# Kernel tuning notes

Hardware: AMD Instinct MI355X
Metric: run time of the kernel (lower is better)

The kernel has to match this reference:

```python
import jax, jax.numpy as jnp
import numpy as np

N = 100000
E = 1600000
IN_C, HID_C, OUT_C = 64, 64, 32


def setup_inputs() -> dict:
    key = jax.random.key(0)
    ks = jax.random.split(key, 8)
    x = jax.random.normal(ks[0], (N, IN_C), dtype=jnp.float32)
    edge_index = jax.random.randint(ks[1], (2, E), 0, N, dtype=jnp.int64)
    # GCNConv weights (glorot-ish scale) and biases
    W1 = jax.random.normal(ks[2], (IN_C, HID_C), dtype=jnp.float32) / np.sqrt(IN_C)
    b1 = jnp.zeros((HID_C,), dtype=jnp.float32)
    W2 = jax.random.normal(ks[3], (HID_C, HID_C), dtype=jnp.float32) / np.sqrt(HID_C)
    b2 = jnp.zeros((HID_C,), dtype=jnp.float32)
    Wlin = jax.random.normal(ks[4], (HID_C, OUT_C), dtype=jnp.float32) / np.sqrt(HID_C)
    blin = jnp.zeros((OUT_C,), dtype=jnp.float32)
    return {"x": x, "edge_index": edge_index, "W1": W1, "b1": b1,
            "W2": W2, "b2": b2, "Wlin": Wlin, "blin": blin}


def _gcn_norm(edge_index):
    # PyG GCNConv default: add self-loops, symmetric normalization.
    loop = jnp.arange(N, dtype=edge_index.dtype)
    row = jnp.concatenate([edge_index[0], loop])  # source nodes [E+N]
    col = jnp.concatenate([edge_index[1], loop])  # target nodes [E+N]
    deg = jax.ops.segment_sum(jnp.ones_like(col, dtype=jnp.float32), col,
                              num_segments=N)
    dinv = jnp.where(deg > 0, deg ** -0.5, 0.0)
    norm = dinv[row] * dinv[col]  # [E+N]
    return row, col, norm


def _gcn_conv(h, W, b, row, col, norm):
    h = h @ W                                  # [N, F_out]
    msg = h[row] * norm[:, None]               # gather + scale, [E+N, F_out]
    out = jax.ops.segment_sum(msg, col, num_segments=N)  # scatter-add
    return out + b


def reference(x, edge_index, W1, b1, W2, b2, Wlin, blin):
    row, col, norm = _gcn_norm(edge_index)
    h = jax.nn.relu(_gcn_conv(x, W1, b1, row, col, norm))
    h = jax.nn.relu(_gcn_conv(h, W2, b2, row, col, norm))
    return h @ Wlin + blin
```

## Files before the change

### kernel.cpp

```cpp
#include <hip/hip_runtime.h>
#include <hip/hip_fp16.h>

#define IN_C 64
#define HID_C 64
#define OUT_C 32
#define S_NODES  512
#define S_CAP  12288
#define CHUNK_E 2048

typedef _Float16 f16_t;
typedef f16_t f16x2 __attribute__((ext_vector_type(2)));

__device__ __forceinline__ float dot2(unsigned int a, f16x2 b, float c) {
#if __has_builtin(__builtin_amdgcn_fdot2)
    return __builtin_amdgcn_fdot2(*(f16x2*)&a, b, c, false);
#else
    float2 af = __half22float2(*(__half2*)&a);
    __half2 bh; *(f16x2*)&bh = b;
    float2 bf = __half22float2(bh);
    return fmaf(af.x, bf.x, fmaf(af.y, bf.y, c));
#endif
}

__global__ void detect_fmt(const int* ei32, int* flag, int n_check) {
    __shared__ int s_any;
    if (threadIdx.x == 0) s_any = 0;
    __syncthreads();
    int any = 0;
    for (int i = threadIdx.x; i < n_check; i += blockDim.x) {
        if (ei32[2 * i + 1] != 0) any = 1;
    }
    if (any) atomicOr(&s_any, 1);
    __syncthreads();
    if (threadIdx.x == 0) *flag = (s_any == 0) ? 1 : 0;
}

__device__ __forceinline__ int ld_edge(const void* ei, int idx, int is64) {
    if (is64) return (int)((const long long*)ei)[idx];
    return ((const int*)ei)[idx];
}

__global__ __launch_bounds__(256) void bin_edges(const void* ei, int E, const int* flag,
                                                 int* bcur, int NB,
                                                 int* __restrict__ staging) {
    __shared__ int cnt[256], boff[256], lcur[256], gbase[256];
    __shared__ int stg[CHUNK_E];
    __shared__ int s_is64;
    int tid = threadIdx.x;
    if (tid == 0) s_is64 = *flag;
    cnt[tid] = 0;
    __syncthreads();
    int is64 = s_is64;
    int e0 = blockIdx.x * CHUNK_E;
    int e1 = min(E, e0 + CHUNK_E);
    for (int e = e0 + tid; e < e1; e += 256) {
        int dst = ld_edge(ei, E + e, is64);
        atomicAdd(&cnt[dst >> 9], 1);
    }
    __syncthreads();
    int v = cnt[tid];
    gbase[tid] = v;
    __syncthreads();
    for (int o = 1; o < 256; o <<= 1) {
        int u = (tid >= o) ? gbase[tid - o] : 0;
        __syncthreads();
        gbase[tid] += u;
        __syncthreads();
    }
    boff[tid] = gbase[tid] - v;
    lcur[tid] = boff[tid];
    __syncthreads();
    for (int e = e0 + tid; e < e1; e += 256) {
        int src = ld_edge(ei, e, is64);
        int dst = ld_edge(ei, E + e, is64);
        int p = atomicAdd(&lcur[dst >> 9], 1);
        stg[p] = src | ((dst & 511) << 17);
    }
    __syncthreads();
    if (tid < NB && cnt[tid] > 0) gbase[tid] = atomicAdd(&bcur[tid], cnt[tid]);
    __syncthreads();
    int sw = tid >> 4, sl = tid & 15;
    for (int b = sw; b < NB; b += 16) {
        int c = cnt[b];
        if (c == 0) continue;
        int o = boff[b], g = gbase[b];
        size_t gb = (size_t)b * S_CAP;
        for (int j = sl; j < c; j += 16) {
            if (g + j < S_CAP) staging[gb + g + j] = stg[o + j];
        }
    }
}

__global__ void scan_bcur(const int* __restrict__ bcur, int* __restrict__ bbase,
                          int* __restrict__ offs, int nb, int n) {
    __shared__ int s[256];
    int tid = threadIdx.x;
    int v = (tid < nb) ? min(bcur[tid], S_CAP) : 0;
    s[tid] = v;
    __syncthreads();
    for (int o = 1; o < 256; o <<= 1) {
        int u = (tid >= o) ? s[tid - o] : 0;
        __syncthreads();
        s[tid] += u;
        __syncthreads();
    }
    if (tid < nb) bbase[tid] = s[tid] - v;
    if (tid == 255) offs[n] = s[255];
}

__global__ __launch_bounds__(256) void place_fine(const int* __restrict__ staging,
                                                  const int* __restrict__ bcur,
                                                  const int* __restrict__ bbase,
                                                  int* __restrict__ offs,
                                                  float* __restrict__ dinv,
                                                  int* __restrict__ rec, int N) {
    __shared__ int sdeg[S_NODES];
    __shared__ int tsum[256];
    __shared__ int curs[S_NODES];
    int tid = threadIdx.x;
    int base = blockIdx.x * S_NODES;
    int nn = min(S_NODES, N - base);
    int cnt = min(bcur[blockIdx.x], S_CAP);
    size_t sb = (size_t)blockIdx.x * S_CAP;
    sdeg[tid] = 0;
    sdeg[tid + 256] = 0;
    __syncthreads();
    for (int j = tid; j < cnt; j += 256) atomicAdd(&sdeg[staging[sb + j] >> 17], 1);
    __syncthreads();
    int d0 = sdeg[2 * tid], d1 = sdeg[2 * tid + 1];
    tsum[tid] = d0 + d1;
    __syncthreads();
    for (int o = 1; o < 256; o <<= 1) {
        int v = (tid >= o) ? tsum[tid - o] : 0;
        __syncthreads();
        tsum[tid] += v;
        __syncthreads();
    }
    int pre = bbase[blockIdx.x] + ((tid == 0) ? 0 : tsum[tid - 1]);
    curs[2 * tid] = pre;
    curs[2 * tid + 1] = pre + d0;
    if (2 * tid < nn) {
        offs[base + 2 * tid] = pre;
        dinv[base + 2 * tid] = rsqrtf((float)(d0 + 1));
    }
    if (2 * tid + 1 < nn) {
        offs[base + 2 * tid + 1] = pre + d0;
        dinv[base + 2 * tid + 1] = rsqrtf((float)(d1 + 1));
    }
    __syncthreads();
    for (int j = tid; j < cnt; j += 256) {
        int pk = staging[sb + j];
        int p = atomicAdd(&curs[pk >> 17], 1);
        rec[p] = pk & 0x1FFFF;
    }
}

__global__ __launch_bounds__(256) void gemm64(const void* __restrict__ in, int in_is_f32,
                                              const float* __restrict__ W,
                                              unsigned short* __restrict__ out,
                                              const float* __restrict__ dinv, int n) {
    __shared__ uint2 sA[32 * 16];
    int tid = threadIdx.x;
    int lane = tid & 63, wave = tid >> 6;
    f16x2 w2[32];
#pragma unroll
    for (int k = 0; k < 32; k++) {
        f16x2 p;
        p.x = (f16_t)W[(2 * k) * 64 + lane];
        p.y = (f16_t)W[(2 * k + 1) * 64 + lane];
        w2[k] = p;
    }
    int base = blockIdx.x * 32;
    if (in_is_f32) {
        const float2* A2 = (const float2*)in;
        int lim = n * 32;
        for (int i = tid; i < 1024; i += 256) {
            int gi = base * 32 + i;
            float2 v = (gi < lim) ? A2[gi] : make_float2(0.f, 0.f);
            ((__half2*)sA)[i] = __floats2half2_rn(v.x, v.y);
        }
    } else {
        const uint2* A2 = (const uint2*)in;
        int lim = n * 16;
        for (int i = tid; i < 512; i += 256) {
            int gi = base * 16 + i;
            sA[i] = (gi < lim) ? A2[gi] : make_uint2(0u, 0u);
        }
    }
    __syncthreads();
    int r0 = base + wave * 8;
    int r1 = min(r0 + 8, n);
    for (int r = r0; r < r1; r++) {
        int rr = r - base;
        float a0 = 0.f, a1 = 0.f;
#pragma unroll
        for (int j = 0; j < 16; j++) {
            uint2 u = sA[rr * 16 + j];
            a0 = dot2(u.x, w2[2 * j], a0);
            a1 = dot2(u.y, w2[2 * j + 1], a1);
        }
        __half hv = __float2half_rn((a0 + a1) * dinv[r]);
        out[(size_t)r * 64 + lane] = *(unsigned short*)&hv;
    }
}

__global__ void aggregate(const unsigned short* __restrict__ t,
                          const int* __restrict__ offs, const int* __restrict__ rec,
                          const float* __restrict__ dinv, const float* __restrict__ bias,
                          unsigned short* __restrict__ acc, int n) {
    int wave = (blockIdx.x * blockDim.x + threadIdx.x) >> 6;
    int lane = threadIdx.x & 63;
    if (wave >= n) return;
    int g = lane >> 3;
    int gl = lane & 7;
    int beg = offs[wave], end = offs[wave + 1];
    int m = end - beg + 1;
    const uint4* t4 = (const uint4*)t;
    float s[8] = {0.f, 0.f, 0.f, 0.f, 0.f, 0.f, 0.f, 0.f};
    for (int i = 0; i < m; i += 32) {
        int srcs[4];
        float ws[4];
#pragma unroll
        for (int u = 0; u < 4; u++) {
            int it = i + u * 8 + g;
            srcs[u] = (it == 0) ? wave : ((it < m) ? rec[beg + it - 1] : wave);
            ws[u] = (it < m) ? 1.f : 0.f;
        }
        uint4 vs[4];
#pragma unroll
        for (int u = 0; u < 4; u++) vs[u] = t4[(size_t)srcs[u] * 8 + gl];
#pragma unroll
        for (int u = 0; u < 4; u++) {
            float w = ws[u];
            float2 f0 = __half22float2(*(__half2*)&vs[u].x);
            float2 f1 = __half22float2(*(__half2*)&vs[u].y);
            float2 f2 = __half22float2(*(__half2*)&vs[u].z);
            float2 f3 = __half22float2(*(__half2*)&vs[u].w);
            s[0] = fmaf(f0.x, w, s[0]);
            s[1] = fmaf(f0.y, w, s[1]);
            s[2] = fmaf(f1.x, w, s[2]);
            s[3] = fmaf(f1.y, w, s[3]);
            s[4] = fmaf(f2.x, w, s[4]);
            s[5] = fmaf(f2.y, w, s[5]);
            s[6] = fmaf(f3.x, w, s[6]);
            s[7] = fmaf(f3.y, w, s[7]);
        }
    }
#pragma unroll
    for (int k = 0; k < 8; k++) {
        s[k] += __shfl_xor(s[k], 8);
        s[k] += __shfl_xor(s[k], 16);
        s[k] += __shfl_xor(s[k], 32);
    }
    if (g == 0) {
        float d = dinv[wave];
        const float4* b4 = (const float4*)bias;
        float4 bb0 = b4[gl * 2], bb1 = b4[gl * 2 + 1];
        float o0 = fmaxf(fmaf(s[0], d, bb0.x), 0.f);
        float o1 = fmaxf(fmaf(s[1], d, bb0.y), 0.f);
        float o2 = fmaxf(fmaf(s[2], d, bb0.z), 0.f);
        float o3 = fmaxf(fmaf(s[3], d, bb0.w), 0.f);
        float o4 = fmaxf(fmaf(s[4], d, bb1.x), 0.f);
        float o5 = fmaxf(fmaf(s[5], d, bb1.y), 0.f);
        float o6 = fmaxf(fmaf(s[6], d, bb1.z), 0.f);
        float o7 = fmaxf(fmaf(s[7], d, bb1.w), 0.f);
        __half2 p0 = __floats2half2_rn(o0, o1);
        __half2 p1 = __floats2half2_rn(o2, o3);
        __half2 p2 = __floats2half2_rn(o4, o5);
        __half2 p3 = __floats2half2_rn(o6, o7);
        ((uint4*)acc)[(size_t)wave * 8 + gl] =
            make_uint4(*(unsigned int*)&p0, *(unsigned int*)&p1,
                       *(unsigned int*)&p2, *(unsigned int*)&p3);
    }
}

__global__ __launch_bounds__(256) void gemm32(const unsigned short* __restrict__ in,
                                              const float* __restrict__ W,
                                              const float* __restrict__ b,
                                              float* __restrict__ out, int n) {
    __shared__ uint2 sA[32 * 16];
    int tid = threadIdx.x;
    int lane = tid & 63, wave = tid >> 6;
    int c = lane & 31;
    f16x2 w2[32];
#pragma unroll
    for (int k = 0; k < 32; k++) {
        f16x2 p;
        p.x = (f16_t)W[(2 * k) * 32 + c];
        p.y = (f16_t)W[(2 * k + 1) * 32 + c];
        w2[k] = p;
    }
    float bl = b[c];
    int base = blockIdx.x * 32;
    const uint2* A2 = (const uint2*)in;
    int lim = n * 16;
    for (int i = tid; i < 512; i += 256) {
        int gi = base * 16 + i;
        sA[i] = (gi < lim) ? A2[gi] : make_uint2(0u, 0u);
    }
    __syncthreads();
    int r0 = base + wave * 8;
    int r1 = min(r0 + 8, n);
    for (int r = r0; r < r1; r++) {
        int rr = r - base;
        float a0 = 0.f, a1 = 0.f;
#pragma unroll
        for (int j = 0; j < 16; j++) {
            uint2 u = sA[rr * 16 + j];
            a0 = dot2(u.x, w2[2 * j], a0);
            a1 = dot2(u.y, w2[2 * j + 1], a1);
        }
        if (lane < 32) out[(size_t)r * 32 + c] = bl + a0 + a1;
    }
}

extern "C" void kernel_launch(void* const* d_in, const int* in_sizes, int n_in,
                              void* d_out, int out_size, void* d_ws, size_t ws_size,
                              hipStream_t stream) {
    (void)n_in; (void)out_size; (void)ws_size;
    const float* x    = (const float*)d_in[0];
    const void*  ei   = d_in[1];
    const float* W1   = (const float*)d_in[2];
    const float* b1   = (const float*)d_in[3];
    const float* W2   = (const float*)d_in[4];
    const float* b2   = (const float*)d_in[5];
    const float* Wlin = (const float*)d_in[6];
    const float* blin = (const float*)d_in[7];
    float* out = (float*)d_out;

    const int N = in_sizes[0] / IN_C;
    const int E = in_sizes[1] / 2;
    const int NB = (N + S_NODES - 1) / S_NODES;
    const int NEB = (E + CHUNK_E - 1) / CHUNK_E;

    char* ws = (char*)d_ws;
    size_t off = 0;
    auto alloc = [&](size_t bytes) -> void* {
        size_t a = (off + 255) & ~(size_t)255;
        off = a + bytes;
        return (void*)(ws + a);
    };
    int*   flag    = (int*)  alloc(4);
    int*   offs    = (int*)  alloc((size_t)(N + 1) * 4);
    float* dinv    = (float*)alloc((size_t)N * 4);
    int*   bcur    = (int*)  alloc((size_t)NB * 4);
    int*   bbase   = (int*)  alloc((size_t)NB * 4);
    int*   rec     = (int*)  alloc((size_t)E * 4);
    int*   staging = (int*)  alloc((size_t)NB * S_CAP * 4);
    unsigned short* tbuf = (unsigned short*)alloc((size_t)N * HID_C * 2);
    unsigned short* acc  = (unsigned short*)alloc((size_t)N * HID_C * 2);

    hipMemsetAsync(bcur, 0, (size_t)NB * 4, stream);

    int n_check = E < 4096 ? E : 4096;
    detect_fmt<<<1, 256, 0, stream>>>((const int*)ei, flag, n_check);
    bin_edges<<<NEB, 256, 0, stream>>>(ei, E, flag, bcur, NB, staging);
    scan_bcur<<<1, 256, 0, stream>>>(bcur, bbase, offs, NB, N);
    place_fine<<<NB, 256, 0, stream>>>(staging, bcur, bbase, offs, dinv, rec, N);

    const int GB = (N + 31) / 32;
    gemm64<<<GB, 256, 0, stream>>>(x, 1, W1, tbuf, dinv, N);
    aggregate<<<(N + 3) / 4, 256, 0, stream>>>(tbuf, offs, rec, dinv, b1, acc, N);
    gemm64<<<GB, 256, 0, stream>>>(acc, 0, W2, tbuf, dinv, N);
    aggregate<<<(N + 3) / 4, 256, 0, stream>>>(tbuf, offs, rec, dinv, b2, acc, N);
    gemm32<<<GB, 256, 0, stream>>>(acc, Wlin, blin, out, N);
}
```

Measured before the change: 267.0 us.

## Fuse aggregation with following GEMM, pre-transpose fp16 weights, merge scan into place

Aggregation is fused with the next layer's dense transform: each wave aggregates a node, stages the row in LDS, and multiplies by the next weight matrix, so the intermediate activation round trip and two GEMM kernels go away. Weights are converted once to fp16 and stored transposed, so GEMM kernels load them with vector loads. The bucket scan is folded into place_fine, which removes a launch. The fused kernels use a persistent grid of 2048 blocks with a grid-stride loop over nodes, which adds register pressure and per-node serial GEMM work inside the latency-bound gather loop.

```diff
diff --git a/kernel.cpp b/kernel.cpp
--- a/kernel.cpp
+++ b/kernel.cpp
@@ -11,18 +11,22 @@
 typedef _Float16 f16_t;
 typedef f16_t f16x2 __attribute__((ext_vector_type(2)));
 
-__device__ __forceinline__ float dot2(unsigned int a, f16x2 b, float c) {
+__device__ __forceinline__ float dot2(unsigned int a, unsigned int b, float c) {
 #if __has_builtin(__builtin_amdgcn_fdot2)
-    return __builtin_amdgcn_fdot2(*(f16x2*)&a, b, c, false);
+    return __builtin_amdgcn_fdot2(*(f16x2*)&a, *(f16x2*)&b, c, false);
 #else
     float2 af = __half22float2(*(__half2*)&a);
-    __half2 bh; *(f16x2*)&bh = b;
-    float2 bf = __half22float2(bh);
+    float2 bf = __half22float2(*(__half2*)&b);
     return fmaf(af.x, bf.x, fmaf(af.y, bf.y, c));
 #endif
 }
 
-__global__ void detect_fmt(const int* ei32, int* flag, int n_check) {
+__global__ void prep(const int* ei32, int* flag, int n_check,
+                     const float* __restrict__ W1, const float* __restrict__ W2,
+                     const float* __restrict__ Wlin,
+                     unsigned short* __restrict__ Wh1,
+                     unsigned short* __restrict__ Wh2,
+                     unsigned short* __restrict__ Whl) {
     __shared__ int s_any;
     if (threadIdx.x == 0) s_any = 0;
     __syncthreads();
@@ -31,6 +35,18 @@
         if (ei32[2 * i + 1] != 0) any = 1;
     }
     if (any) atomicOr(&s_any, 1);
+    for (int i = threadIdx.x; i < 4096; i += 256) {
+        int r = i >> 6, c = i & 63;
+        f16_t h1 = (f16_t)W1[r * 64 + c];
+        f16_t h2 = (f16_t)W2[r * 64 + c];
+        Wh1[c * 64 + r] = *(unsigned short*)&h1;
+        Wh2[c * 64 + r] = *(unsigned short*)&h2;
+    }
+    for (int i = threadIdx.x; i < 2048; i += 256) {
+        int r = i >> 5, c = i & 31;
+        f16_t h = (f16_t)Wlin[r * 32 + c];
+        Whl[c * 64 + r] = *(unsigned short*)&h;
+    }
     __syncthreads();
     if (threadIdx.x == 0) *flag = (s_any == 0) ? 1 : 0;
 }
@@ -91,41 +107,34 @@
     }
 }
 
-__global__ void scan_bcur(const int* __restrict__ bcur, int* __restrict__ bbase,
-                          int* __restrict__ offs, int nb, int n) {
-    __shared__ int s[256];
-    int tid = threadIdx.x;
-    int v = (tid < nb) ? min(bcur[tid], S_CAP) : 0;
-    s[tid] = v;
-    __syncthreads();
-    for (int o = 1; o < 256; o <<= 1) {
-        int u = (tid >= o) ? s[tid - o] : 0;
-        __syncthreads();
-        s[tid] += u;
-        __syncthreads();
-    }
-    if (tid < nb) bbase[tid] = s[tid] - v;
-    if (tid == 255) offs[n] = s[255];
-}
-
 __global__ __launch_bounds__(256) void place_fine(const int* __restrict__ staging,
                                                   const int* __restrict__ bcur,
-                                                  const int* __restrict__ bbase,
                                                   int* __restrict__ offs,
                                                   float* __restrict__ dinv,
-                                                  int* __restrict__ rec, int N) {
+                                                  int* __restrict__ rec, int N, int NB) {
     __shared__ int sdeg[S_NODES];
     __shared__ int tsum[256];
     __shared__ int curs[S_NODES];
+    __shared__ int sb[256];
     int tid = threadIdx.x;
+    int vcnt = (tid < NB) ? min(bcur[tid], S_CAP) : 0;
+    sb[tid] = vcnt;
+    sdeg[tid] = 0;
+    sdeg[tid + 256] = 0;
+    __syncthreads();
+    for (int o = 1; o < 256; o <<= 1) {
+        int u = (tid >= o) ? sb[tid - o] : 0;
+        __syncthreads();
+        sb[tid] += u;
+        __syncthreads();
+    }
+    int cnt = min(bcur[blockIdx.x], S_CAP);
+    int bbase = sb[blockIdx.x] - cnt;
+    if (blockIdx.x == NB - 1 && tid == 0) offs[N] = sb[255];
     int base = blockIdx.x * S_NODES;
     int nn = min(S_NODES, N - base);
-    int cnt = min(bcur[blockIdx.x], S_CAP);
-    size_t sb = (size_t)blockIdx.x * S_CAP;
-    sdeg[tid] = 0;
-    sdeg[tid + 256] = 0;
-    __syncthreads();
-    for (int j = tid; j < cnt; j += 256) atomicAdd(&sdeg[staging[sb + j] >> 17], 1);
+    size_t sbase = (size_t)blockIdx.x * S_CAP;
+    for (int j = tid; j < cnt; j += 256) atomicAdd(&sdeg[staging[sbase + j] >> 17], 1);
     __syncthreads();
     int d0 = sdeg[2 * tid], d1 = sdeg[2 * tid + 1];
     tsum[tid] = d0 + d1;
@@ -136,7 +145,7 @@
         tsum[tid] += v;
         __syncthreads();
     }
-    int pre = bbase[blockIdx.x] + ((tid == 0) ? 0 : tsum[tid - 1]);
+    int pre = bbase + ((tid == 0) ? 0 : tsum[tid - 1]);
     curs[2 * tid] = pre;
     curs[2 * tid + 1] = pre + d0;
     if (2 * tid < nn) {
@@ -149,43 +158,36 @@
     }
     __syncthreads();
     for (int j = tid; j < cnt; j += 256) {
-        int pk = staging[sb + j];
+        int pk = staging[sbase + j];
         int p = atomicAdd(&curs[pk >> 17], 1);
         rec[p] = pk & 0x1FFFF;
     }
 }
 
-__global__ __launch_bounds__(256) void gemm64(const void* __restrict__ in, int in_is_f32,
-                                              const float* __restrict__ W,
+__global__ __launch_bounds__(256) void gemm64(const float* __restrict__ in,
+                                              const unsigned short* __restrict__ Wh,
                                               unsigned short* __restrict__ out,
                                               const float* __restrict__ dinv, int n) {
-    __shared__ uint2 sA[32 * 16];
+    __shared__ uint4 sA[32 * 8];
     int tid = threadIdx.x;
     int lane = tid & 63, wave = tid >> 6;
-    f16x2 w2[32];
-#pragma unroll
-    for (int k = 0; k < 32; k++) {
-        f16x2 p;
-        p.x = (f16_t)W[(2 * k) * 64 + lane];
-        p.y = (f16_t)W[(2 * k + 1) * 64 + lane];
-        w2[k] = p;
+    unsigned int wu[32];
+    {
+        const uint4* col = (const uint4*)(Wh + (size_t)lane * 64);
+#pragma unroll
+        for (int j = 0; j < 8; j++) {
+            uint4 w4 = col[j];
+            wu[4 * j] = w4.x; wu[4 * j + 1] = w4.y;
+            wu[4 * j + 2] = w4.z; wu[4 * j + 3] = w4.w;
+        }
     }
     int base = blockIdx.x * 32;
-    if (in_is_f32) {
-        const float2* A2 = (const float2*)in;
-        int lim = n * 32;
-        for (int i = tid; i < 1024; i += 256) {
-            int gi = base * 32 + i;
-            float2 v = (gi < lim) ? A2[gi] : make_float2(0.f, 0.f);
-            ((__half2*)sA)[i] = __floats2half2_rn(v.x, v.y);
-        }
-    } else {
-        const uint2* A2 = (const uint2*)in;
-        int lim = n * 16;
-        for (int i = tid; i < 512; i += 256) {
-            int gi = base * 16 + i;
-            sA[i] = (gi < lim) ? A2[gi] : make_uint2(0u, 0u);
-        }
+    const float2* A2 = (const float2*)in;
+    int lim = n * 32;
+    for (int i = tid; i < 1024; i += 256) {
+        int gi = base * 32 + i;
+        float2 v = (gi < lim) ? A2[gi] : make_float2(0.f, 0.f);
+        ((__half2*)sA)[i] = __floats2half2_rn(v.x, v.y);
     }
     __syncthreads();
     int r0 = base + wave * 8;
@@ -194,123 +196,129 @@
         int rr = r - base;
         float a0 = 0.f, a1 = 0.f;
 #pragma unroll
-        for (int j = 0; j < 16; j++) {
-            uint2 u = sA[rr * 16 + j];
-            a0 = dot2(u.x, w2[2 * j], a0);
-            a1 = dot2(u.y, w2[2 * j + 1], a1);
+        for (int j = 0; j < 8; j++) {
+            uint4 u = sA[rr * 8 + j];
+            a0 = dot2(u.x, wu[4 * j], a0);
+            a1 = dot2(u.y, wu[4 * j + 1], a1);
+            a0 = dot2(u.z, wu[4 * j + 2], a0);
+            a1 = dot2(u.w, wu[4 * j + 3], a1);
         }
         __half hv = __float2half_rn((a0 + a1) * dinv[r]);
         out[(size_t)r * 64 + lane] = *(unsigned short*)&hv;
     }
 }
 
-__global__ void aggregate(const unsigned short* __restrict__ t,
-                          const int* __restrict__ offs, const int* __restrict__ rec,
-                          const float* __restrict__ dinv, const float* __restrict__ bias,
-                          unsigned short* __restrict__ acc, int n) {
-    int wave = (blockIdx.x * blockDim.x + threadIdx.x) >> 6;
-    int lane = threadIdx.x & 63;
-    if (wave >= n) return;
+template <int MODE>
+__global__ __launch_bounds__(256) void agg_gemm(const unsigned short* __restrict__ t,
+                                                const int* __restrict__ offs,
+                                                const int* __restrict__ rec,
+                                                const float* __restrict__ dinv,
+                                                const float* __restrict__ bias,
+                                                const unsigned short* __restrict__ Wh,
+                                                unsigned short* __restrict__ outh,
+                                                float* __restrict__ outf,
+                                                const float* __restrict__ blin, int n) {
+    constexpr int COLS = (MODE == 0) ? 64 : 32;
+    __shared__ unsigned short sW[64 * COLS];
+    __shared__ uint4 srow[4][8];
+    int tid = threadIdx.x;
+    int lane = tid & 63, wave = tid >> 6;
+    {
+        const uint4* s4 = (const uint4*)Wh;
+        uint4* d4 = (uint4*)sW;
+        for (int i = tid; i < 64 * COLS / 8; i += 256) d4[i] = s4[i];
+    }
+    __syncthreads();
+    int c = (MODE == 0) ? lane : (lane & 31);
+    unsigned int wu[32];
+    {
+        const uint4* col = ((const uint4*)sW) + c * 8;
+#pragma unroll
+        for (int j = 0; j < 8; j++) {
+            uint4 w4 = col[j];
+            wu[4 * j] = w4.x; wu[4 * j + 1] = w4.y;
+            wu[4 * j + 2] = w4.z; wu[4 * j + 3] = w4.w;
+        }
+    }
     int g = lane >> 3;
     int gl = lane & 7;
-    int beg = offs[wave], end = offs[wave + 1];
-    int m = end - beg + 1;
+    const float4* b4 = (const float4*)bias;
+    float4 bb0 = b4[gl * 2], bb1 = b4[gl * 2 + 1];
+    float bl = (MODE == 1) ? blin[c] : 0.f;
     const uint4* t4 = (const uint4*)t;
-    float s[8] = {0.f, 0.f, 0.f, 0.f, 0.f, 0.f, 0.f, 0.f};
-    for (int i = 0; i < m; i += 32) {
-        int srcs[4];
-        float ws[4];
-#pragma unroll
-        for (int u = 0; u < 4; u++) {
-            int it = i + u * 8 + g;
-            srcs[u] = (it == 0) ? wave : ((it < m) ? rec[beg + it - 1] : wave);
-            ws[u] = (it < m) ? 1.f : 0.f;
-        }
-        uint4 vs[4];
-#pragma unroll
-        for (int u = 0; u < 4; u++) vs[u] = t4[(size_t)srcs[u] * 8 + gl];
-#pragma unroll
-        for (int u = 0; u < 4; u++) {
-            float w = ws[u];
-            float2 f0 = __half22float2(*(__half2*)&vs[u].x);
-            float2 f1 = __half22float2(*(__half2*)&vs[u].y);
-            float2 f2 = __half22float2(*(__half2*)&vs[u].z);
-            float2 f3 = __half22float2(*(__half2*)&vs[u].w);
-            s[0] = fmaf(f0.x, w, s[0]);
-            s[1] = fmaf(f0.y, w, s[1]);
-            s[2] = fmaf(f1.x, w, s[2]);
-            s[3] = fmaf(f1.y, w, s[3]);
-            s[4] = fmaf(f2.x, w, s[4]);
-            s[5] = fmaf(f2.y, w, s[5]);
-            s[6] = fmaf(f3.x, w, s[6]);
-            s[7] = fmaf(f3.y, w, s[7]);
-        }
-    }
-#pragma unroll
-    for (int k = 0; k < 8; k++) {
-        s[k] += __shfl_xor(s[k], 8);
-        s[k] += __shfl_xor(s[k], 16);
-        s[k] += __shfl_xor(s[k], 32);
-    }
-    if (g == 0) {
-        float d = dinv[wave];
-        const float4* b4 = (const float4*)bias;
-        float4 bb0 = b4[gl * 2], bb1 = b4[gl * 2 + 1];
-        float o0 = fmaxf(fmaf(s[0], d, bb0.x), 0.f);
-        float o1 = fmaxf(fmaf(s[1], d, bb0.y), 0.f);
-        float o2 = fmaxf(fmaf(s[2], d, bb0.z), 0.f);
-        float o3 = fmaxf(fmaf(s[3], d, bb0.w), 0.f);
-        float o4 = fmaxf(fmaf(s[4], d, bb1.x), 0.f);
-        float o5 = fmaxf(fmaf(s[5], d, bb1.y), 0.f);
-        float o6 = fmaxf(fmaf(s[6], d, bb1.z), 0.f);
-        float o7 = fmaxf(fmaf(s[7], d, bb1.w), 0.f);
-        __half2 p0 = __floats2half2_rn(o0, o1);
-        __half2 p1 = __floats2half2_rn(o2, o3);
-        __half2 p2 = __floats2half2_rn(o4, o5);
-        __half2 p3 = __floats2half2_rn(o6, o7);
-        ((uint4*)acc)[(size_t)wave * 8 + gl] =
-            make_uint4(*(unsigned int*)&p0, *(unsigned int*)&p1,
-                       *(unsigned int*)&p2, *(unsigned int*)&p3);
-    }
-}
-
-__global__ __launch_bounds__(256) void gemm32(const unsigned short* __restrict__ in,
-                                              const float* __restrict__ W,
-                                              const float* __restrict__ b,
-                                              float* __restrict__ out, int n) {
-    __shared__ uint2 sA[32 * 16];
-    int tid = threadIdx.x;
-    int lane = tid & 63, wave = tid >> 6;
-    int c = lane & 31;
-    f16x2 w2[32];
-#pragma unroll
-    for (int k = 0; k < 32; k++) {
-        f16x2 p;
-        p.x = (f16_t)W[(2 * k) * 32 + c];
-        p.y = (f16_t)W[(2 * k + 1) * 32 + c];
-        w2[k] = p;
-    }
-    float bl = b[c];
-    int base = blockIdx.x * 32;
-    const uint2* A2 = (const uint2*)in;
-    int lim = n * 16;
-    for (int i = tid; i < 512; i += 256) {
-        int gi = base * 16 + i;
-        sA[i] = (gi < lim) ? A2[gi] : make_uint2(0u, 0u);
-    }
-    __syncthreads();
-    int r0 = base + wave * 8;
-    int r1 = min(r0 + 8, n);
-    for (int r = r0; r < r1; r++) {
-        int rr = r - base;
+    int nw = gridDim.x * 4;
+    for (int node = blockIdx.x * 4 + wave; node < n; node += nw) {
+        int beg = offs[node], end = offs[node + 1];
+        int m = end - beg + 1;
+        float s[8] = {0.f, 0.f, 0.f, 0.f, 0.f, 0.f, 0.f, 0.f};
+        for (int i = 0; i < m; i += 32) {
+            int srcs[4];
+            float ws[4];
+#pragma unroll
+            for (int u = 0; u < 4; u++) {
+                int it = i + u * 8 + g;
+                srcs[u] = (it == 0) ? node : ((it < m) ? rec[beg + it - 1] : node);
+                ws[u] = (it < m) ? 1.f : 0.f;
+            }
+            uint4 vs[4];
+#pragma unroll
+            for (int u = 0; u < 4; u++) vs[u] = t4[(size_t)srcs[u] * 8 + gl];
+#pragma unroll
+            for (int u = 0; u < 4; u++) {
+                float w = ws[u];
+                float2 f0 = __half22float2(*(__half2*)&vs[u].x);
+                float2 f1 = __half22float2(*(__half2*)&vs[u].y);
+                float2 f2 = __half22float2(*(__half2*)&vs[u].z);
+                float2 f3 = __half22float2(*(__half2*)&vs[u].w);
+                s[0] = fmaf(f0.x, w, s[0]);
+                s[1] = fmaf(f0.y, w, s[1]);
+                s[2] = fmaf(f1.x, w, s[2]);
+                s[3] = fmaf(f1.y, w, s[3]);
+                s[4] = fmaf(f2.x, w, s[4]);
+                s[5] = fmaf(f2.y, w, s[5]);
+                s[6] = fmaf(f3.x, w, s[6]);
+                s[7] = fmaf(f3.y, w, s[7]);
+            }
+        }
+#pragma unroll
+        for (int k = 0; k < 8; k++) {
+            s[k] += __shfl_xor(s[k], 8);
+            s[k] += __shfl_xor(s[k], 16);
+            s[k] += __shfl_xor(s[k], 32);
+        }
+        float d = dinv[node];
+        if (g == 0) {
+            float o0 = fmaxf(fmaf(s[0], d, bb0.x), 0.f);
+            float o1 = fmaxf(fmaf(s[1], d, bb0.y), 0.f);
+            float o2 = fmaxf(fmaf(s[2], d, bb0.z), 0.f);
+            float o3 = fmaxf(fmaf(s[3], d, bb0.w), 0.f);
+            float o4 = fmaxf(fmaf(s[4], d, bb1.x), 0.f);
+            float o5 = fmaxf(fmaf(s[5], d, bb1.y), 0.f);
+            float o6 = fmaxf(fmaf(s[6], d, bb1.z), 0.f);
+            float o7 = fmaxf(fmaf(s[7], d, bb1.w), 0.f);
+            __half2 p0 = __floats2half2_rn(o0, o1);
+            __half2 p1 = __floats2half2_rn(o2, o3);
+            __half2 p2 = __floats2half2_rn(o4, o5);
+            __half2 p3 = __floats2half2_rn(o6, o7);
+            srow[wave][gl] = make_uint4(*(unsigned int*)&p0, *(unsigned int*)&p1,
+                                        *(unsigned int*)&p2, *(unsigned int*)&p3);
+        }
         float a0 = 0.f, a1 = 0.f;
 #pragma unroll
-        for (int j = 0; j < 16; j++) {
-            uint2 u = sA[rr * 16 + j];
-            a0 = dot2(u.x, w2[2 * j], a0);
-            a1 = dot2(u.y, w2[2 * j + 1], a1);
-        }
-        if (lane < 32) out[(size_t)r * 32 + c] = bl + a0 + a1;
+        for (int j = 0; j < 8; j++) {
+            uint4 u = srow[wave][j];
+            a0 = dot2(u.x, wu[4 * j], a0);
+            a1 = dot2(u.y, wu[4 * j + 1], a1);
+            a0 = dot2(u.z, wu[4 * j + 2], a0);
+            a1 = dot2(u.w, wu[4 * j + 3], a1);
+        }
+        float val = a0 + a1;
+        if (MODE == 0) {
+            __half hv = __float2half_rn(val * d);
+            outh[(size_t)node * 64 + lane] = *(unsigned short*)&hv;
+        } else {
+            if (lane < 32) outf[(size_t)node * 32 + c] = bl + val;
+        }
     }
 }
 
@@ -344,24 +352,29 @@
     int*   offs    = (int*)  alloc((size_t)(N + 1) * 4);
     float* dinv    = (float*)alloc((size_t)N * 4);
     int*   bcur    = (int*)  alloc((size_t)NB * 4);
-    int*   bbase   = (int*)  alloc((size_t)NB * 4);
     int*   rec     = (int*)  alloc((size_t)E * 4);
     int*   staging = (int*)  alloc((size_t)NB * S_CAP * 4);
     unsigned short* tbuf = (unsigned short*)alloc((size_t)N * HID_C * 2);
     unsigned short* acc  = (unsigned short*)alloc((size_t)N * HID_C * 2);
+    unsigned short* Wh1  = (unsigned short*)alloc(64 * 64 * 2);
+    unsigned short* Wh2  = (unsigned short*)alloc(64 * 64 * 2);
+    unsigned short* Whl  = (unsigned short*)alloc(64 * 32 * 2);
 
     hipMemsetAsync(bcur, 0, (size_t)NB * 4, stream);
 
     int n_check = E < 4096 ? E : 4096;
-    detect_fmt<<<1, 256, 0, stream>>>((const int*)ei, flag, n_check);
+    prep<<<1, 256, 0, stream>>>((const int*)ei, flag, n_check, W1, W2, Wlin,
+                                Wh1, Wh2, Whl);
     bin_edges<<<NEB, 256, 0, stream>>>(ei, E, flag, bcur, NB, staging);
-    scan_bcur<<<1, 256, 0, stream>>>(bcur, bbase, offs, NB, N);
-    place_fine<<<NB, 256, 0, stream>>>(staging, bcur, bbase, offs, dinv, rec, N);
+    place_fine<<<NB, 256, 0, stream>>>(staging, bcur, offs, dinv, rec, N, NB);
 
     const int GB = (N + 31) / 32;
-    gemm64<<<GB, 256, 0, stream>>>(x, 1, W1, tbuf, dinv, N);
-    aggregate<<<(N + 3) / 4, 256, 0, stream>>>(tbuf, offs, rec, dinv, b1, acc, N);
-    gemm64<<<GB, 256, 0, stream>>>(acc, 0, W2, tbuf, dinv, N);
-    aggregate<<<(N + 3) / 4, 256, 0, stream>>>(tbuf, offs, rec, dinv, b2, acc, N);
-    gemm32<<<GB, 256, 0, stream>>>(acc, Wlin, blin, out, N);
-}
+    gemm64<<<GB, 256, 0, stream>>>(x, Wh1, tbuf, dinv, N);
+
+    int AG = 2048;
+    if (AG * 4 > N) AG = (N + 3) / 4;
+    agg_gemm<0><<<AG, 256, 0, stream>>>(tbuf, offs, rec, dinv, b1, Wh2,
+                                        acc, nullptr, nullptr, N);
+    agg_gemm<1><<<AG, 256, 0, stream>>>(acc, offs, rec, dinv, b2, Whl,
+                                        nullptr, out, blin, N);
+}
```

Result: slower. 289.0 us (+8.2%).
